# Kernel optimization log

Hardware: AMD Instinct MI355X
Metric: run time of the kernel (lower is better)

The kernel has to match this reference:

```python
import jax, jax.numpy as jnp
import numpy as np

D_IN = 256
H = 512


def _linear_params(key, fan_in, fan_out):
    kw, kb = jax.random.split(key)
    bound = 1.0 / np.sqrt(fan_in)
    W = jax.random.uniform(kw, (fan_in, fan_out), minval=-bound, maxval=bound, dtype=jnp.float32)
    b = jax.random.uniform(kb, (fan_out,), minval=-bound, maxval=bound, dtype=jnp.float32)
    return W, b


def setup_inputs() -> dict:
    key = jax.random.key(0)
    ks = jax.random.split(key, 7)
    brick_vectors = jax.random.normal(ks[0], (8, 128, D_IN), dtype=jnp.float32)
    Wa, ba = _linear_params(ks[1], D_IN, H)
    Wb, bb = _linear_params(ks[2], H, H)
    Wca, bca = _linear_params(ks[3], 2 * H, H)
    Wcb, bcb = _linear_params(ks[4], H, H)
    Wcc, bcc = _linear_params(ks[5], H, H)
    Wo, bo = _linear_params(ks[6], H, 2)
    return {
        "brick_vectors": brick_vectors,
        "Wa": Wa, "ba": ba,
        "Wb": Wb, "bb": bb,
        "Wca": Wca, "bca": bca,
        "Wcb": Wcb, "bcb": bcb,
        "Wcc": Wcc, "bcc": bcc,
        "Wo": Wo, "bo": bo,
    }


def reference(brick_vectors, Wa, ba, Wb, bb, Wca, bca, Wcb, bcb, Wcc, bcc, Wo, bo):
    B, N, _ = brick_vectors.shape
    x = brick_vectors.reshape(-1, D_IN)            # [B*N, D_IN]
    f = jax.nn.relu(x @ Wa + ba)                   # node MLP
    f = jax.nn.relu(f @ Wb + bb)                   # [B*N, 512]
    f = f.reshape(B, N, H)
    # pairwise broadcast-concat: pair (i, j) gets cat(f[:, j], f[:, i])
    fa = jnp.broadcast_to(f[:, None, :, :], (B, N, N, H))   # varies over j (last pair axis)
    fb = jnp.broadcast_to(f[:, :, None, :], (B, N, N, H))   # varies over i
    e = jnp.concatenate((fa, fb), axis=-1).reshape(-1, 2 * H)  # [B*N*N, 1024]
    e = jax.nn.relu(e @ Wca + bca)
    e = jax.nn.relu(e @ Wcb + bcb)
    e = jax.nn.relu(e @ Wcc + bcc)
    out = e @ Wo + bo                               # [B*N*N, 2]
    return out.reshape(B, N, N, 2)
```

## Files before the change

kernel.cpp:

```cpp
#include <hip/hip_runtime.h>

typedef __bf16 bf16x8 __attribute__((ext_vector_type(8)));
typedef float f32x16 __attribute__((ext_vector_type(16)));

#define GLOAD_LDS16(gsrc, ldst)                                                   \
  __builtin_amdgcn_global_load_lds(                                               \
      (const __attribute__((address_space(1))) void*)(gsrc),                      \
      (__attribute__((address_space(3))) void*)(ldst), 16, 0, 0)

__global__ __launch_bounds__(256) void prep_pack(const float* __restrict__ Wcb,
                                                 const float* __restrict__ Wcc,
                                                 __bf16* __restrict__ Pb,
                                                 __bf16* __restrict__ Pc) {
  int idx = blockIdx.x * 256 + threadIdx.x;
  const float* src = (idx < 262144) ? Wcb : Wcc;
  __bf16* dst = (idx < 262144) ? Pb : Pc;
  int t = idx & 262143;
  int e = t & 7, l = (t >> 3) & 63, kb = (t >> 9) & 31, c = t >> 14;
  int k = kb * 16 + ((l >> 5) << 3) + e;
  int n = (c << 5) + (l & 31);
  dst[t] = (__bf16)src[k * 512 + n];
}

__global__ __launch_bounds__(256) void gemm_f32(const float* __restrict__ A,
                                                const float* __restrict__ W,
                                                const float* __restrict__ bias,
                                                float* __restrict__ C,
                                                int K, int N, int do_relu) {
  __shared__ float As[16][68];
  __shared__ float Ws[16][32];
  int bm = blockIdx.x * 64, bn = blockIdx.y * 32;
  int tid = threadIdx.x;
  int tx = tid & 15, ty = tid >> 4;
  float acc[4][2] = {};
  for (int k0 = 0; k0 < K; k0 += 16) {
#pragma unroll
    for (int ii = 0; ii < 4; ii++) {
      int e = ii * 256 + tid; int r = e >> 4, c = e & 15;
      As[c][r] = A[(bm + r) * K + k0 + c];
    }
#pragma unroll
    for (int ii = 0; ii < 2; ii++) {
      int e = ii * 256 + tid; int kr = e >> 5, c = e & 31;
      Ws[kr][c] = W[(k0 + kr) * N + bn + c];
    }
    __syncthreads();
#pragma unroll
    for (int kk = 0; kk < 16; kk++) {
      float4 a = *(const float4*)&As[kk][ty * 4];
      float2 w = *(const float2*)&Ws[kk][tx * 2];
      acc[0][0] += a.x * w.x; acc[0][1] += a.x * w.y;
      acc[1][0] += a.y * w.x; acc[1][1] += a.y * w.y;
      acc[2][0] += a.z * w.x; acc[2][1] += a.z * w.y;
      acc[3][0] += a.w * w.x; acc[3][1] += a.w * w.y;
    }
    __syncthreads();
  }
#pragma unroll
  for (int mi = 0; mi < 4; mi++)
#pragma unroll
    for (int ni = 0; ni < 2; ni++) {
      int n = bn + tx * 2 + ni;
      float vv = acc[mi][ni] + (bias ? bias[n] : 0.f);
      if (do_relu) vv = fmaxf(vv, 0.f);
      C[(bm + ty * 4 + mi) * N + n] = vv;
    }
}

__global__ __launch_bounds__(256) void gemm_uv(const float* __restrict__ A,
                                               const float* __restrict__ Wca,
                                               float* __restrict__ u,
                                               float* __restrict__ v) {
  __shared__ float As[16][68];
  __shared__ float Ws[16][32];
  int half = blockIdx.y >> 4;
  const float* W = Wca + half * 512 * 512;
  float* C = half ? v : u;
  int bm = blockIdx.x * 64, bn = (blockIdx.y & 15) * 32;
  int tid = threadIdx.x;
  int tx = tid & 15, ty = tid >> 4;
  float acc[4][2] = {};
  for (int k0 = 0; k0 < 512; k0 += 16) {
#pragma unroll
    for (int ii = 0; ii < 4; ii++) {
      int e = ii * 256 + tid; int r = e >> 4, c = e & 15;
      As[c][r] = A[(bm + r) * 512 + k0 + c];
    }
#pragma unroll
    for (int ii = 0; ii < 2; ii++) {
      int e = ii * 256 + tid; int kr = e >> 5, c = e & 31;
      Ws[kr][c] = W[(k0 + kr) * 512 + bn + c];
    }
    __syncthreads();
#pragma unroll
    for (int kk = 0; kk < 16; kk++) {
      float4 a = *(const float4*)&As[kk][ty * 4];
      float2 w = *(const float2*)&Ws[kk][tx * 2];
      acc[0][0] += a.x * w.x; acc[0][1] += a.x * w.y;
      acc[1][0] += a.y * w.x; acc[1][1] += a.y * w.y;
      acc[2][0] += a.z * w.x; acc[2][1] += a.z * w.y;
      acc[3][0] += a.w * w.x; acc[3][1] += a.w * w.y;
    }
    __syncthreads();
  }
#pragma unroll
  for (int mi = 0; mi < 4; mi++)
#pragma unroll
    for (int ni = 0; ni < 2; ni++)
      C[(bm + ty * 4 + mi) * 512 + bn + tx * 2 + ni] = acc[mi][ni];
}

__global__ __launch_bounds__(512, 2) void edge_kernel(
    const float* __restrict__ u, const float* __restrict__ v,
    const bf16x8* __restrict__ Pb, const bf16x8* __restrict__ Pc,
    const float* __restrict__ bca, const float* __restrict__ bcb,
    const float* __restrict__ bcc, const float* __restrict__ Wo,
    const float* __restrict__ bo, float* __restrict__ out) {
  __shared__ __align__(16) char h_raw[163840];
  char* Bst = h_raw + 131072;

  int wg = blockIdx.x;
  int i = wg & 127, b = wg >> 7;
  int tid = threadIdx.x, lane = tid & 63, w = tid >> 6;

  int mrow = (w & 1) * 32;
  int n0 = (w >> 1) * 128;
  int cg4 = (w >> 1) * 4;
  int arow = mrow + (lane & 31);
  int sA = (arow & 15) << 4;
  int klo = (lane >> 5) * 8;
  int cb0 = 2 * w;

#define STAGE_B(P, kb, sel)                                                       \
  {                                                                               \
    const char* _g0 = (const char*)((P) + (cb0 * 32 + (kb)) * 64) + lane * 16;    \
    const char* _g1 = (const char*)((P) + ((cb0 + 1) * 32 + (kb)) * 64) + lane * 16; \
    GLOAD_LDS16(_g0, Bst + (sel) * 16384 + cb0 * 1024);                           \
    GLOAD_LDS16(_g1, Bst + (sel) * 16384 + (cb0 + 1) * 1024);                     \
  }

  STAGE_B(Pb, 0, 0)

  {
    int k2 = tid & 255;
    float2 vv = *(const float2*)(v + (b * 128 + i) * 512 + 2 * k2);
    float2 bc = *(const float2*)(bca + 2 * k2);
    float vb0 = vv.x + bc.x, vb1 = vv.y + bc.y;
    const float* ub = u + (b * 128) * 512;
#pragma unroll 4
    for (int it = 0; it < 64; it++) {
      int r = it * 2 + (tid >> 8);
      float2 uu = *(const float2*)(ub + r * 512 + 2 * k2);
      float x0 = fmaxf(uu.x + vb0, 0.f);
      float x1 = fmaxf(uu.y + vb1, 0.f);
      unsigned short s0 = __builtin_bit_cast(unsigned short, (__bf16)x0);
      unsigned short s1 = __builtin_bit_cast(unsigned short, (__bf16)x1);
      unsigned int pk = ((unsigned int)s1 << 16) | (unsigned int)s0;
      int rt = r & 63;
      int wbyte = ((r >> 6) << 16) + rt * 1024 + ((4 * k2) ^ ((rt & 15) << 4));
      *(unsigned int*)(h_raw + wbyte) = pk;
    }
  }
  __syncthreads();

  f32x16 acc0[4], acc1[4];

#pragma unroll
  for (int nb = 0; nb < 4; nb++)
#pragma unroll
    for (int r = 0; r < 16; r++) { acc0[nb][r] = 0.f; acc1[nb][r] = 0.f; }
#pragma unroll 2
  for (int kb = 0; kb < 32; kb++) {
    int sel = kb & 1;
    if (kb < 31) STAGE_B(Pb, kb + 1, sel ^ 1)
    const char* bb = Bst + sel * 16384 + lane * 16;
    bf16x8 b0 = *(const bf16x8*)(bb + (cg4 + 0) * 1024);
    bf16x8 b1 = *(const bf16x8*)(bb + (cg4 + 1) * 1024);
    bf16x8 b2 = *(const bf16x8*)(bb + (cg4 + 2) * 1024);
    bf16x8 b3 = *(const bf16x8*)(bb + (cg4 + 3) * 1024);
    int abyte = arow * 1024 + (((kb * 16 + klo) * 2) ^ sA);
    bf16x8 a0 = *(const bf16x8*)(h_raw + abyte);
    bf16x8 a1 = *(const bf16x8*)(h_raw + 65536 + abyte);
    acc0[0] = __builtin_amdgcn_mfma_f32_32x32x16_bf16(a0, b0, acc0[0], 0, 0, 0);
    acc1[0] = __builtin_amdgcn_mfma_f32_32x32x16_bf16(a1, b0, acc1[0], 0, 0, 0);
    acc0[1] = __builtin_amdgcn_mfma_f32_32x32x16_bf16(a0, b1, acc0[1], 0, 0, 0);
    acc1[1] = __builtin_amdgcn_mfma_f32_32x32x16_bf16(a1, b1, acc1[1], 0, 0, 0);
    acc0[2] = __builtin_amdgcn_mfma_f32_32x32x16_bf16(a0, b2, acc0[2], 0, 0, 0);
    acc1[2] = __builtin_amdgcn_mfma_f32_32x32x16_bf16(a1, b2, acc1[2], 0, 0, 0);
    acc0[3] = __builtin_amdgcn_mfma_f32_32x32x16_bf16(a0, b3, acc0[3], 0, 0, 0);
    acc1[3] = __builtin_amdgcn_mfma_f32_32x32x16_bf16(a1, b3, acc1[3], 0, 0, 0);
    __syncthreads();
  }
  STAGE_B(Pc, 0, 0)

#pragma unroll
  for (int nb = 0; nb < 4; nb++) {
    int cn = n0 + nb * 32 + (lane & 31);
    float bbv = bcb[cn];
#pragma unroll
    for (int r = 0; r < 16; r++) {
      int row = mrow + (r & 3) + 8 * (r >> 2) + 4 * (lane >> 5);
      int byte_ = row * 1024 + ((cn * 2) ^ ((row & 15) << 4));
      *(__bf16*)(h_raw + byte_) = (__bf16)fmaxf(acc0[nb][r] + bbv, 0.f);
      *(__bf16*)(h_raw + 65536 + byte_) = (__bf16)fmaxf(acc1[nb][r] + bbv, 0.f);
    }
  }
  __syncthreads();

#pragma unroll
  for (int nb = 0; nb < 4; nb++)
#pragma unroll
    for (int r = 0; r < 16; r++) { acc0[nb][r] = 0.f; acc1[nb][r] = 0.f; }
#pragma unroll 2
  for (int kb = 0; kb < 32; kb++) {
    int sel = kb & 1;
    if (kb < 31) STAGE_B(Pc, kb + 1, sel ^ 1)
    const char* bb = Bst + sel * 16384 + lane * 16;
    bf16x8 b0 = *(const bf16x8*)(bb + (cg4 + 0) * 1024);
    bf16x8 b1 = *(const bf16x8*)(bb + (cg4 + 1) * 1024);
    bf16x8 b2 = *(const bf16x8*)(bb + (cg4 + 2) * 1024);
    bf16x8 b3 = *(const bf16x8*)(bb + (cg4 + 3) * 1024);
    int abyte = arow * 1024 + (((kb * 16 + klo) * 2) ^ sA);
    bf16x8 a0 = *(const bf16x8*)(h_raw + abyte);
    bf16x8 a1 = *(const bf16x8*)(h_raw + 65536 + abyte);
    acc0[0] = __builtin_amdgcn_mfma_f32_32x32x16_bf16(a0, b0, acc0[0], 0, 0, 0);
    acc1[0] = __builtin_amdgcn_mfma_f32_32x32x16_bf16(a1, b0, acc1[0], 0, 0, 0);
    acc0[1] = __builtin_amdgcn_mfma_f32_32x32x16_bf16(a0, b1, acc0[1], 0, 0, 0);
    acc1[1] = __builtin_amdgcn_mfma_f32_32x32x16_bf16(a1, b1, acc1[1], 0, 0, 0);
    acc0[2] = __builtin_amdgcn_mfma_f32_32x32x16_bf16(a0, b2, acc0[2], 0, 0, 0);
    acc1[2] = __builtin_amdgcn_mfma_f32_32x32x16_bf16(a1, b2, acc1[2], 0, 0, 0);
    acc0[3] = __builtin_amdgcn_mfma_f32_32x32x16_bf16(a0, b3, acc0[3], 0, 0, 0);
    acc1[3] = __builtin_amdgcn_mfma_f32_32x32x16_bf16(a1, b3, acc1[3], 0, 0, 0);
    __syncthreads();
  }

  float p0[16][2] = {}, p1[16][2] = {};
#pragma unroll
  for (int nb = 0; nb < 4; nb++) {
    int cn = n0 + nb * 32 + (lane & 31);
    float bcv = bcc[cn];
    float2 wov = *(const float2*)(Wo + cn * 2);
#pragma unroll
    for (int r = 0; r < 16; r++) {
      float h30 = fmaxf(acc0[nb][r] + bcv, 0.f);
      float h31 = fmaxf(acc1[nb][r] + bcv, 0.f);
      p0[r][0] += h30 * wov.x; p0[r][1] += h30 * wov.y;
      p1[r][0] += h31 * wov.x; p1[r][1] += h31 * wov.y;
    }
  }
#pragma unroll
  for (int m = 1; m <= 16; m <<= 1) {
#pragma unroll
    for (int r = 0; r < 16; r++) {
      p0[r][0] += __shfl_xor(p0[r][0], m, 64);
      p0[r][1] += __shfl_xor(p0[r][1], m, 64);
      p1[r][0] += __shfl_xor(p1[r][0], m, 64);
      p1[r][1] += __shfl_xor(p1[r][1], m, 64);
    }
  }
  __syncthreads();
  float* red = (float*)h_raw;
  if ((lane & 31) == 0) {
    int hh = lane >> 5, cg = w >> 1;
#pragma unroll
    for (int r = 0; r < 16; r++) {
      int row = mrow + (r & 3) + 8 * (r >> 2) + 4 * hh;
      red[(cg * 128 + row) * 2 + 0] = p0[r][0];
      red[(cg * 128 + row) * 2 + 1] = p0[r][1];
      red[(cg * 128 + 64 + row) * 2 + 0] = p1[r][0];
      red[(cg * 128 + 64 + row) * 2 + 1] = p1[r][1];
    }
  }
  __syncthreads();
  if (tid < 256) {
    int row = tid >> 1, d = tid & 1;
    float s = red[(0 * 128 + row) * 2 + d] + red[(1 * 128 + row) * 2 + d] +
              red[(2 * 128 + row) * 2 + d] + red[(3 * 128 + row) * 2 + d] + bo[d];
    out[((b * 128 + i) * 128 + row) * 2 + d] = s;
  }
#undef STAGE_B
}

extern "C" void kernel_launch(void* const* d_in, const int* in_sizes, int n_in,
                              void* d_out, int out_size, void* d_ws, size_t ws_size,
                              hipStream_t stream) {
  const float* x   = (const float*)d_in[0];
  const float* Wa  = (const float*)d_in[1];
  const float* ba  = (const float*)d_in[2];
  const float* Wb  = (const float*)d_in[3];
  const float* bb  = (const float*)d_in[4];
  const float* Wca = (const float*)d_in[5];
  const float* bca = (const float*)d_in[6];
  const float* Wcb = (const float*)d_in[7];
  const float* bcb = (const float*)d_in[8];
  const float* Wcc = (const float*)d_in[9];
  const float* bcc = (const float*)d_in[10];
  const float* Wo  = (const float*)d_in[11];
  const float* bo  = (const float*)d_in[12];
  float* out = (float*)d_out;

  char* ws = (char*)d_ws;
  float* f1 = (float*)(ws);
  float* f  = (float*)(ws + (2u << 20));
  float* u  = (float*)(ws + (4u << 20));
  float* v  = (float*)(ws + (6u << 20));
  __bf16* Pb = (__bf16*)(ws + (8u << 20));
  __bf16* Pc = (__bf16*)(ws + (8u << 20) + (512u << 10));

  prep_pack<<<2048, 256, 0, stream>>>(Wcb, Wcc, Pb, Pc);
  gemm_f32<<<dim3(16, 16), 256, 0, stream>>>(x, Wa, ba, f1, 256, 512, 1);
  gemm_f32<<<dim3(16, 16), 256, 0, stream>>>(f1, Wb, bb, f, 512, 512, 1);
  gemm_uv<<<dim3(16, 32), 256, 0, stream>>>(f, Wca, u, v);
  edge_kernel<<<1024, 512, 0, stream>>>(u, v, (const bf16x8*)Pb, (const bf16x8*)Pc,
                                        bca, bcb, bcc, Wo, bo, out);
}
```

Before: 255.6 us.

## Split edge tiles to 64 rows, 4-slot B prefetch with fine-grained waitcnt

Each workgroup now handles 64 j-rows instead of 128, doubling the grid to 2048 blocks and shrinking LDS use from 160KB to 128KB. Each wave now owns 64 output columns (two 32-wide blocks) rather than 128, so it holds four accumulators instead of eight. Weight staging moves to a 4-slot ring with a prefetch distance of two, explicit vmcnt waits and raw s_barrier instead of __syncthreads, and s_setprio around the MFMAs. This targets the per-k-step sync stalls and aims for better latency hiding. The cost is that each block streams the full weight matrices for only half the rows, which doubles weight traffic per output.

```diff
diff --git a/kernel.cpp b/kernel.cpp
--- a/kernel.cpp
+++ b/kernel.cpp
@@ -116,39 +116,54 @@
     const float* __restrict__ bca, const float* __restrict__ bcb,
     const float* __restrict__ bcc, const float* __restrict__ Wo,
     const float* __restrict__ bo, float* __restrict__ out) {
-  __shared__ __align__(16) char h_raw[163840];
-  char* Bst = h_raw + 131072;
+  __shared__ __align__(16) char h_raw[131072];
+  char* Bst = h_raw + 65536;
 
   int wg = blockIdx.x;
-  int i = wg & 127, b = wg >> 7;
+  int jh = wg & 1, i = (wg >> 1) & 127, b = wg >> 8;
+  int j0 = jh * 64;
   int tid = threadIdx.x, lane = tid & 63, w = tid >> 6;
 
-  int mrow = (w & 1) * 32;
-  int n0 = (w >> 1) * 128;
-  int cg4 = (w >> 1) * 4;
-  int arow = mrow + (lane & 31);
-  int sA = (arow & 15) << 4;
+  int cb0 = 2 * w;
+  int r0 = lane & 31;
+  int sA = (r0 & 15) << 4;
   int klo = (lane >> 5) * 8;
-  int cb0 = 2 * w;
-
-#define STAGE_B(P, kb, sel)                                                       \
+
+#define STAGE_B(P, kb, slot)                                                      \
   {                                                                               \
-    const char* _g0 = (const char*)((P) + (cb0 * 32 + (kb)) * 64) + lane * 16;    \
-    const char* _g1 = (const char*)((P) + ((cb0 + 1) * 32 + (kb)) * 64) + lane * 16; \
-    GLOAD_LDS16(_g0, Bst + (sel) * 16384 + cb0 * 1024);                           \
-    GLOAD_LDS16(_g1, Bst + (sel) * 16384 + (cb0 + 1) * 1024);                     \
-  }
-
-  STAGE_B(Pb, 0, 0)
+    const char* g0_ = (const char*)((P) + ((cb0) * 32 + (kb)) * 64) + lane * 16;  \
+    const char* g1_ = (const char*)((P) + ((cb0 + 1) * 32 + (kb)) * 64) + lane * 16; \
+    GLOAD_LDS16(g0_, Bst + (slot) * 16384 + (cb0) * 1024);                        \
+    GLOAD_LDS16(g1_, Bst + (slot) * 16384 + (cb0 + 1) * 1024);                    \
+  }
+
+#define KSTEP(P, kb, DO_STAGE, VMSTR)                                             \
+  {                                                                               \
+    if (DO_STAGE) STAGE_B(P, (kb) + 2, ((kb) + 2) & 3)                            \
+    const char* bb_ = Bst + ((kb) & 3) * 16384 + lane * 16;                       \
+    bf16x8 b0 = *(const bf16x8*)(bb_ + cb0 * 1024);                               \
+    bf16x8 b1 = *(const bf16x8*)(bb_ + (cb0 + 1) * 1024);                         \
+    int ab_ = (((kb) * 16 + klo) * 2) ^ sA;                                       \
+    bf16x8 a0 = *(const bf16x8*)(h_raw + r0 * 1024 + ab_);                        \
+    bf16x8 a1 = *(const bf16x8*)(h_raw + (r0 + 32) * 1024 + ab_);                 \
+    __builtin_amdgcn_s_setprio(1);                                                \
+    accA0 = __builtin_amdgcn_mfma_f32_32x32x16_bf16(a0, b0, accA0, 0, 0, 0);      \
+    accA1 = __builtin_amdgcn_mfma_f32_32x32x16_bf16(a0, b1, accA1, 0, 0, 0);      \
+    accB0 = __builtin_amdgcn_mfma_f32_32x32x16_bf16(a1, b0, accB0, 0, 0, 0);      \
+    accB1 = __builtin_amdgcn_mfma_f32_32x32x16_bf16(a1, b1, accB1, 0, 0, 0);      \
+    __builtin_amdgcn_s_setprio(0);                                                \
+    asm volatile("s_waitcnt vmcnt(" VMSTR ")" ::: "memory");                      \
+    __builtin_amdgcn_s_barrier();                                                 \
+  }
 
   {
     int k2 = tid & 255;
     float2 vv = *(const float2*)(v + (b * 128 + i) * 512 + 2 * k2);
     float2 bc = *(const float2*)(bca + 2 * k2);
     float vb0 = vv.x + bc.x, vb1 = vv.y + bc.y;
-    const float* ub = u + (b * 128) * 512;
+    const float* ub = u + (b * 128 + j0) * 512;
 #pragma unroll 4
-    for (int it = 0; it < 64; it++) {
+    for (int it = 0; it < 32; it++) {
       int r = it * 2 + (tid >> 8);
       float2 uu = *(const float2*)(ub + r * 512 + 2 * k2);
       float x0 = fmaxf(uu.x + vb0, 0.f);
@@ -156,94 +171,63 @@
       unsigned short s0 = __builtin_bit_cast(unsigned short, (__bf16)x0);
       unsigned short s1 = __builtin_bit_cast(unsigned short, (__bf16)x1);
       unsigned int pk = ((unsigned int)s1 << 16) | (unsigned int)s0;
-      int rt = r & 63;
-      int wbyte = ((r >> 6) << 16) + rt * 1024 + ((4 * k2) ^ ((rt & 15) << 4));
+      int wbyte = r * 1024 + ((4 * k2) ^ ((r & 15) << 4));
       *(unsigned int*)(h_raw + wbyte) = pk;
     }
   }
-  __syncthreads();
-
-  f32x16 acc0[4], acc1[4];
-
-#pragma unroll
-  for (int nb = 0; nb < 4; nb++)
-#pragma unroll
-    for (int r = 0; r < 16; r++) { acc0[nb][r] = 0.f; acc1[nb][r] = 0.f; }
-#pragma unroll 2
-  for (int kb = 0; kb < 32; kb++) {
-    int sel = kb & 1;
-    if (kb < 31) STAGE_B(Pb, kb + 1, sel ^ 1)
-    const char* bb = Bst + sel * 16384 + lane * 16;
-    bf16x8 b0 = *(const bf16x8*)(bb + (cg4 + 0) * 1024);
-    bf16x8 b1 = *(const bf16x8*)(bb + (cg4 + 1) * 1024);
-    bf16x8 b2 = *(const bf16x8*)(bb + (cg4 + 2) * 1024);
-    bf16x8 b3 = *(const bf16x8*)(bb + (cg4 + 3) * 1024);
-    int abyte = arow * 1024 + (((kb * 16 + klo) * 2) ^ sA);
-    bf16x8 a0 = *(const bf16x8*)(h_raw + abyte);
-    bf16x8 a1 = *(const bf16x8*)(h_raw + 65536 + abyte);
-    acc0[0] = __builtin_amdgcn_mfma_f32_32x32x16_bf16(a0, b0, acc0[0], 0, 0, 0);
-    acc1[0] = __builtin_amdgcn_mfma_f32_32x32x16_bf16(a1, b0, acc1[0], 0, 0, 0);
-    acc0[1] = __builtin_amdgcn_mfma_f32_32x32x16_bf16(a0, b1, acc0[1], 0, 0, 0);
-    acc1[1] = __builtin_amdgcn_mfma_f32_32x32x16_bf16(a1, b1, acc1[1], 0, 0, 0);
-    acc0[2] = __builtin_amdgcn_mfma_f32_32x32x16_bf16(a0, b2, acc0[2], 0, 0, 0);
-    acc1[2] = __builtin_amdgcn_mfma_f32_32x32x16_bf16(a1, b2, acc1[2], 0, 0, 0);
-    acc0[3] = __builtin_amdgcn_mfma_f32_32x32x16_bf16(a0, b3, acc0[3], 0, 0, 0);
-    acc1[3] = __builtin_amdgcn_mfma_f32_32x32x16_bf16(a1, b3, acc1[3], 0, 0, 0);
-    __syncthreads();
-  }
+
+  f32x16 accA0, accA1, accB0, accB1;
+#pragma unroll
+  for (int r = 0; r < 16; r++) { accA0[r] = 0.f; accA1[r] = 0.f; accB0[r] = 0.f; accB1[r] = 0.f; }
+
+  asm volatile("s_waitcnt vmcnt(0)" ::: "memory");
+  STAGE_B(Pb, 0, 0)
+  STAGE_B(Pb, 1, 1)
+  asm volatile("s_waitcnt vmcnt(2) lgkmcnt(0)" ::: "memory");
+  __builtin_amdgcn_s_barrier();
+
+  for (int kb = 0; kb < 30; kb++) KSTEP(Pb, kb, 1, "2")
+  KSTEP(Pb, 30, 0, "0")
+  KSTEP(Pb, 31, 0, "0")
+
   STAGE_B(Pc, 0, 0)
-
-#pragma unroll
-  for (int nb = 0; nb < 4; nb++) {
-    int cn = n0 + nb * 32 + (lane & 31);
+  STAGE_B(Pc, 1, 1)
+
+#pragma unroll
+  for (int blk = 0; blk < 2; blk++) {
+    int cn = (cb0 + blk) * 32 + (lane & 31);
     float bbv = bcb[cn];
+    const f32x16& A0 = blk ? accA1 : accA0;
+    const f32x16& A1 = blk ? accB1 : accB0;
 #pragma unroll
     for (int r = 0; r < 16; r++) {
-      int row = mrow + (r & 3) + 8 * (r >> 2) + 4 * (lane >> 5);
-      int byte_ = row * 1024 + ((cn * 2) ^ ((row & 15) << 4));
-      *(__bf16*)(h_raw + byte_) = (__bf16)fmaxf(acc0[nb][r] + bbv, 0.f);
-      *(__bf16*)(h_raw + 65536 + byte_) = (__bf16)fmaxf(acc1[nb][r] + bbv, 0.f);
-    }
-  }
-  __syncthreads();
-
-#pragma unroll
-  for (int nb = 0; nb < 4; nb++)
-#pragma unroll
-    for (int r = 0; r < 16; r++) { acc0[nb][r] = 0.f; acc1[nb][r] = 0.f; }
-#pragma unroll 2
-  for (int kb = 0; kb < 32; kb++) {
-    int sel = kb & 1;
-    if (kb < 31) STAGE_B(Pc, kb + 1, sel ^ 1)
-    const char* bb = Bst + sel * 16384 + lane * 16;
-    bf16x8 b0 = *(const bf16x8*)(bb + (cg4 + 0) * 1024);
-    bf16x8 b1 = *(const bf16x8*)(bb + (cg4 + 1) * 1024);
-    bf16x8 b2 = *(const bf16x8*)(bb + (cg4 + 2) * 1024);
-    bf16x8 b3 = *(const bf16x8*)(bb + (cg4 + 3) * 1024);
-    int abyte = arow * 1024 + (((kb * 16 + klo) * 2) ^ sA);
-    bf16x8 a0 = *(const bf16x8*)(h_raw + abyte);
-    bf16x8 a1 = *(const bf16x8*)(h_raw + 65536 + abyte);
-    acc0[0] = __builtin_amdgcn_mfma_f32_32x32x16_bf16(a0, b0, acc0[0], 0, 0, 0);
-    acc1[0] = __builtin_amdgcn_mfma_f32_32x32x16_bf16(a1, b0, acc1[0], 0, 0, 0);
-    acc0[1] = __builtin_amdgcn_mfma_f32_32x32x16_bf16(a0, b1, acc0[1], 0, 0, 0);
-    acc1[1] = __builtin_amdgcn_mfma_f32_32x32x16_bf16(a1, b1, acc1[1], 0, 0, 0);
-    acc0[2] = __builtin_amdgcn_mfma_f32_32x32x16_bf16(a0, b2, acc0[2], 0, 0, 0);
-    acc1[2] = __builtin_amdgcn_mfma_f32_32x32x16_bf16(a1, b2, acc1[2], 0, 0, 0);
-    acc0[3] = __builtin_amdgcn_mfma_f32_32x32x16_bf16(a0, b3, acc0[3], 0, 0, 0);
-    acc1[3] = __builtin_amdgcn_mfma_f32_32x32x16_bf16(a1, b3, acc1[3], 0, 0, 0);
-    __syncthreads();
-  }
+      int crow = (r & 3) + 8 * (r >> 2) + 4 * (lane >> 5);
+      int byte_ = crow * 1024 + ((cn * 2) ^ ((crow & 15) << 4));
+      *(__bf16*)(h_raw + byte_) = (__bf16)fmaxf(A0[r] + bbv, 0.f);
+      *(__bf16*)(h_raw + byte_ + 32 * 1024) = (__bf16)fmaxf(A1[r] + bbv, 0.f);
+    }
+  }
+#pragma unroll
+  for (int r = 0; r < 16; r++) { accA0[r] = 0.f; accA1[r] = 0.f; accB0[r] = 0.f; accB1[r] = 0.f; }
+  asm volatile("s_waitcnt vmcnt(2) lgkmcnt(0)" ::: "memory");
+  __builtin_amdgcn_s_barrier();
+
+  for (int kb = 0; kb < 30; kb++) KSTEP(Pc, kb, 1, "2")
+  KSTEP(Pc, 30, 0, "0")
+  KSTEP(Pc, 31, 0, "0")
 
   float p0[16][2] = {}, p1[16][2] = {};
 #pragma unroll
-  for (int nb = 0; nb < 4; nb++) {
-    int cn = n0 + nb * 32 + (lane & 31);
+  for (int blk = 0; blk < 2; blk++) {
+    int cn = (cb0 + blk) * 32 + (lane & 31);
     float bcv = bcc[cn];
     float2 wov = *(const float2*)(Wo + cn * 2);
+    const f32x16& A0 = blk ? accA1 : accA0;
+    const f32x16& A1 = blk ? accB1 : accB0;
 #pragma unroll
     for (int r = 0; r < 16; r++) {
-      float h30 = fmaxf(acc0[nb][r] + bcv, 0.f);
-      float h31 = fmaxf(acc1[nb][r] + bcv, 0.f);
+      float h30 = fmaxf(A0[r] + bcv, 0.f);
+      float h31 = fmaxf(A1[r] + bcv, 0.f);
       p0[r][0] += h30 * wov.x; p0[r][1] += h30 * wov.y;
       p1[r][0] += h31 * wov.x; p1[r][1] += h31 * wov.y;
     }
@@ -261,23 +245,25 @@
   __syncthreads();
   float* red = (float*)h_raw;
   if ((lane & 31) == 0) {
-    int hh = lane >> 5, cg = w >> 1;
+    int hh = lane >> 5;
 #pragma unroll
     for (int r = 0; r < 16; r++) {
-      int row = mrow + (r & 3) + 8 * (r >> 2) + 4 * hh;
-      red[(cg * 128 + row) * 2 + 0] = p0[r][0];
-      red[(cg * 128 + row) * 2 + 1] = p0[r][1];
-      red[(cg * 128 + 64 + row) * 2 + 0] = p1[r][0];
-      red[(cg * 128 + 64 + row) * 2 + 1] = p1[r][1];
+      int crow = (r & 3) + 8 * (r >> 2) + 4 * hh;
+      red[(w * 64 + crow) * 2 + 0] = p0[r][0];
+      red[(w * 64 + crow) * 2 + 1] = p0[r][1];
+      red[(w * 64 + 32 + crow) * 2 + 0] = p1[r][0];
+      red[(w * 64 + 32 + crow) * 2 + 1] = p1[r][1];
     }
   }
   __syncthreads();
-  if (tid < 256) {
+  if (tid < 128) {
     int row = tid >> 1, d = tid & 1;
-    float s = red[(0 * 128 + row) * 2 + d] + red[(1 * 128 + row) * 2 + d] +
-              red[(2 * 128 + row) * 2 + d] + red[(3 * 128 + row) * 2 + d] + bo[d];
-    out[((b * 128 + i) * 128 + row) * 2 + d] = s;
-  }
+    float s = bo[d];
+#pragma unroll
+    for (int ww = 0; ww < 8; ww++) s += red[(ww * 64 + row) * 2 + d];
+    out[(((b * 128 + i) * 128) + j0 + row) * 2 + d] = s;
+  }
+#undef KSTEP
 #undef STAGE_B
 }
 
@@ -311,6 +297,6 @@
   gemm_f32<<<dim3(16, 16), 256, 0, stream>>>(x, Wa, ba, f1, 256, 512, 1);
   gemm_f32<<<dim3(16, 16), 256, 0, stream>>>(f1, Wb, bb, f, 512, 512, 1);
   gemm_uv<<<dim3(16, 32), 256, 0, stream>>>(f, Wca, u, v);
-  edge_kernel<<<1024, 512, 0, stream>>>(u, v, (const bf16x8*)Pb, (const bf16x8*)Pc,
+  edge_kernel<<<2048, 512, 0, stream>>>(u, v, (const bf16x8*)Pb, (const bf16x8*)Pc,
                                         bca, bcb, bcc, Wo, bo, out);
 }
```

Measured after the change: 302.5 us. 1.18x slower.

## Replace scalar fp32 node GEMMs with bf16 MFMA kernels using packed weights

Applied to the files above, without the earlier changes.

The three fp32 SIMT GEMMs for the node MLP and the u/v projection are replaced by a templated bf16 MFMA kernel. It stages activations into swizzled LDS and reads weights prepacked into MFMA fragment order. All weight packing now happens in one larger pack kernel. This cuts per-node GEMM compute time but only launches 16–32 blocks of 512 threads, and lowers node-feature precision to bf16.

```diff
diff --git a/kernel.cpp b/kernel.cpp
--- a/kernel.cpp
+++ b/kernel.cpp
@@ -8,106 +8,115 @@
       (const __attribute__((address_space(1))) void*)(gsrc),                      \
       (__attribute__((address_space(3))) void*)(ldst), 16, 0, 0)
 
-__global__ __launch_bounds__(256) void prep_pack(const float* __restrict__ Wcb,
-                                                 const float* __restrict__ Wcc,
-                                                 __bf16* __restrict__ Pb,
-                                                 __bf16* __restrict__ Pc) {
-  int idx = blockIdx.x * 256 + threadIdx.x;
-  const float* src = (idx < 262144) ? Wcb : Wcc;
-  __bf16* dst = (idx < 262144) ? Pb : Pc;
-  int t = idx & 262143;
-  int e = t & 7, l = (t >> 3) & 63, kb = (t >> 9) & 31, c = t >> 14;
+__device__ __forceinline__ void pack_one(const float* __restrict__ src,
+                                         __bf16* __restrict__ dst,
+                                         int t, int kbshift) {
+  int e = t & 7, l = (t >> 3) & 63;
+  int kb = (t >> 9) & ((1 << kbshift) - 1);
+  int c = t >> (9 + kbshift);
   int k = kb * 16 + ((l >> 5) << 3) + e;
   int n = (c << 5) + (l & 31);
   dst[t] = (__bf16)src[k * 512 + n];
 }
 
-__global__ __launch_bounds__(256) void gemm_f32(const float* __restrict__ A,
-                                                const float* __restrict__ W,
-                                                const float* __restrict__ bias,
-                                                float* __restrict__ C,
-                                                int K, int N, int do_relu) {
-  __shared__ float As[16][68];
-  __shared__ float Ws[16][32];
-  int bm = blockIdx.x * 64, bn = blockIdx.y * 32;
-  int tid = threadIdx.x;
-  int tx = tid & 15, ty = tid >> 4;
-  float acc[4][2] = {};
-  for (int k0 = 0; k0 < K; k0 += 16) {
-#pragma unroll
-    for (int ii = 0; ii < 4; ii++) {
-      int e = ii * 256 + tid; int r = e >> 4, c = e & 15;
-      As[c][r] = A[(bm + r) * K + k0 + c];
-    }
-#pragma unroll
-    for (int ii = 0; ii < 2; ii++) {
-      int e = ii * 256 + tid; int kr = e >> 5, c = e & 31;
-      Ws[kr][c] = W[(k0 + kr) * N + bn + c];
-    }
-    __syncthreads();
-#pragma unroll
-    for (int kk = 0; kk < 16; kk++) {
-      float4 a = *(const float4*)&As[kk][ty * 4];
-      float2 w = *(const float2*)&Ws[kk][tx * 2];
-      acc[0][0] += a.x * w.x; acc[0][1] += a.x * w.y;
-      acc[1][0] += a.y * w.x; acc[1][1] += a.y * w.y;
-      acc[2][0] += a.z * w.x; acc[2][1] += a.z * w.y;
-      acc[3][0] += a.w * w.x; acc[3][1] += a.w * w.y;
-    }
-    __syncthreads();
-  }
-#pragma unroll
-  for (int mi = 0; mi < 4; mi++)
-#pragma unroll
-    for (int ni = 0; ni < 2; ni++) {
-      int n = bn + tx * 2 + ni;
-      float vv = acc[mi][ni] + (bias ? bias[n] : 0.f);
-      if (do_relu) vv = fmaxf(vv, 0.f);
-      C[(bm + ty * 4 + mi) * N + n] = vv;
-    }
-}
-
-__global__ __launch_bounds__(256) void gemm_uv(const float* __restrict__ A,
-                                               const float* __restrict__ Wca,
-                                               float* __restrict__ u,
-                                               float* __restrict__ v) {
-  __shared__ float As[16][68];
-  __shared__ float Ws[16][32];
-  int half = blockIdx.y >> 4;
-  const float* W = Wca + half * 512 * 512;
-  float* C = half ? v : u;
-  int bm = blockIdx.x * 64, bn = (blockIdx.y & 15) * 32;
-  int tid = threadIdx.x;
-  int tx = tid & 15, ty = tid >> 4;
-  float acc[4][2] = {};
-  for (int k0 = 0; k0 < 512; k0 += 16) {
-#pragma unroll
-    for (int ii = 0; ii < 4; ii++) {
-      int e = ii * 256 + tid; int r = e >> 4, c = e & 15;
-      As[c][r] = A[(bm + r) * 512 + k0 + c];
-    }
-#pragma unroll
-    for (int ii = 0; ii < 2; ii++) {
-      int e = ii * 256 + tid; int kr = e >> 5, c = e & 31;
-      Ws[kr][c] = W[(k0 + kr) * 512 + bn + c];
-    }
-    __syncthreads();
-#pragma unroll
-    for (int kk = 0; kk < 16; kk++) {
-      float4 a = *(const float4*)&As[kk][ty * 4];
-      float2 w = *(const float2*)&Ws[kk][tx * 2];
-      acc[0][0] += a.x * w.x; acc[0][1] += a.x * w.y;
-      acc[1][0] += a.y * w.x; acc[1][1] += a.y * w.y;
-      acc[2][0] += a.z * w.x; acc[2][1] += a.z * w.y;
-      acc[3][0] += a.w * w.x; acc[3][1] += a.w * w.y;
-    }
-    __syncthreads();
-  }
-#pragma unroll
-  for (int mi = 0; mi < 4; mi++)
-#pragma unroll
-    for (int ni = 0; ni < 2; ni++)
-      C[(bm + ty * 4 + mi) * 512 + bn + tx * 2 + ni] = acc[mi][ni];
+__global__ __launch_bounds__(256) void pack_all(
+    const float* __restrict__ Wcb, const float* __restrict__ Wcc,
+    const float* __restrict__ Wb, const float* __restrict__ Wca,
+    const float* __restrict__ Wa,
+    __bf16* __restrict__ Pb, __bf16* __restrict__ Pc,
+    __bf16* __restrict__ PWb, __bf16* __restrict__ PH0,
+    __bf16* __restrict__ PH1, __bf16* __restrict__ PWa) {
+  int idx = blockIdx.x * 256 + threadIdx.x;
+  if (idx < 262144) {
+    pack_one(Wcb, Pb, idx, 5);
+  } else if (idx < 524288) {
+    pack_one(Wcc, Pc, idx - 262144, 5);
+  } else if (idx < 786432) {
+    pack_one(Wb, PWb, idx - 524288, 5);
+  } else if (idx < 1048576) {
+    pack_one(Wca, PH0, idx - 786432, 5);
+  } else if (idx < 1310720) {
+    pack_one(Wca + 512 * 512, PH1, idx - 1048576, 5);
+  } else if (idx < 1441792) {
+    pack_one(Wa, PWa, idx - 1310720, 4);
+  }
+}
+
+template <int K>
+__global__ __launch_bounds__(512, 2) void node_mfma(
+    const float* __restrict__ A, const bf16x8* __restrict__ P0,
+    const bf16x8* __restrict__ P1, const float* __restrict__ bias,
+    int do_relu, float* __restrict__ C0, float* __restrict__ C1) {
+  constexpr int KB = K / 16;
+  constexpr int KH = K / 2;
+  __shared__ __align__(16) char sA[64 * K * 2];
+
+  int row0 = blockIdx.x * 64;
+  const bf16x8* P = blockIdx.y ? P1 : P0;
+  float* C = blockIdx.y ? C1 : C0;
+  int tid = threadIdx.x, lane = tid & 63, w = tid >> 6;
+
+  {
+    int k2 = tid & (KH - 1);
+    int rof = tid / KH;
+    constexpr int RPI = 512 / KH;
+#pragma unroll 4
+    for (int it = 0; it < 64 / RPI; it++) {
+      int r = it * RPI + rof;
+      float2 aa = *(const float2*)(A + (row0 + r) * K + 2 * k2);
+      unsigned short s0 = __builtin_bit_cast(unsigned short, (__bf16)aa.x);
+      unsigned short s1 = __builtin_bit_cast(unsigned short, (__bf16)aa.y);
+      unsigned int pk = ((unsigned int)s1 << 16) | (unsigned int)s0;
+      int wbyte = r * (2 * K) + ((4 * k2) ^ ((r & 15) << 4));
+      *(unsigned int*)(sA + wbyte) = pk;
+    }
+  }
+  __syncthreads();
+
+  int mrow = (w & 1) * 32;
+  int n0 = (w >> 1) * 128;
+  int cg4 = (w >> 1) * 4;
+  int arow = mrow + (lane & 31);
+  int sAk = (arow & 15) << 4;
+  int klo = (lane >> 5) * 8;
+
+  const bf16x8* B0 = P + ((cg4 + 0) * KB) * 64 + lane;
+  const bf16x8* B1 = P + ((cg4 + 1) * KB) * 64 + lane;
+  const bf16x8* B2 = P + ((cg4 + 2) * KB) * 64 + lane;
+  const bf16x8* B3 = P + ((cg4 + 3) * KB) * 64 + lane;
+
+  f32x16 acc[4];
+#pragma unroll
+  for (int nb = 0; nb < 4; nb++)
+#pragma unroll
+    for (int r = 0; r < 16; r++) acc[nb][r] = 0.f;
+
+#pragma unroll 2
+  for (int kb = 0; kb < KB; kb++) {
+    int abyte = arow * (2 * K) + (((kb * 16 + klo) * 2) ^ sAk);
+    bf16x8 a = *(const bf16x8*)(sA + abyte);
+    bf16x8 b0 = B0[kb * 64];
+    bf16x8 b1 = B1[kb * 64];
+    bf16x8 b2 = B2[kb * 64];
+    bf16x8 b3 = B3[kb * 64];
+    acc[0] = __builtin_amdgcn_mfma_f32_32x32x16_bf16(a, b0, acc[0], 0, 0, 0);
+    acc[1] = __builtin_amdgcn_mfma_f32_32x32x16_bf16(a, b1, acc[1], 0, 0, 0);
+    acc[2] = __builtin_amdgcn_mfma_f32_32x32x16_bf16(a, b2, acc[2], 0, 0, 0);
+    acc[3] = __builtin_amdgcn_mfma_f32_32x32x16_bf16(a, b3, acc[3], 0, 0, 0);
+  }
+
+#pragma unroll
+  for (int nb = 0; nb < 4; nb++) {
+    int cn = n0 + nb * 32 + (lane & 31);
+    float bv = bias ? bias[cn] : 0.f;
+#pragma unroll
+    for (int r = 0; r < 16; r++) {
+      int rr = mrow + (r & 3) + 8 * (r >> 2) + 4 * (lane >> 5);
+      float val = acc[nb][r] + bv;
+      if (do_relu) val = fmaxf(val, 0.f);
+      C[(row0 + rr) * 512 + cn] = val;
+    }
+  }
 }
 
 __global__ __launch_bounds__(512, 2) void edge_kernel(
@@ -304,13 +313,21 @@
   float* f  = (float*)(ws + (2u << 20));
   float* u  = (float*)(ws + (4u << 20));
   float* v  = (float*)(ws + (6u << 20));
-  __bf16* Pb = (__bf16*)(ws + (8u << 20));
-  __bf16* Pc = (__bf16*)(ws + (8u << 20) + (512u << 10));
-
-  prep_pack<<<2048, 256, 0, stream>>>(Wcb, Wcc, Pb, Pc);
-  gemm_f32<<<dim3(16, 16), 256, 0, stream>>>(x, Wa, ba, f1, 256, 512, 1);
-  gemm_f32<<<dim3(16, 16), 256, 0, stream>>>(f1, Wb, bb, f, 512, 512, 1);
-  gemm_uv<<<dim3(16, 32), 256, 0, stream>>>(f, Wca, u, v);
+  __bf16* Pb  = (__bf16*)(ws + (8u << 20));
+  __bf16* Pc  = (__bf16*)(ws + (8u << 20) + (512u << 10));
+  __bf16* PWb = (__bf16*)(ws + (9u << 20));
+  __bf16* PH0 = (__bf16*)(ws + (9u << 20) + (512u << 10));
+  __bf16* PH1 = (__bf16*)(ws + (10u << 20));
+  __bf16* PWa = (__bf16*)(ws + (10u << 20) + (512u << 10));
+
+  pack_all<<<5632, 256, 0, stream>>>(Wcb, Wcc, Wb, Wca, Wa,
+                                     Pb, Pc, PWb, PH0, PH1, PWa);
+  node_mfma<256><<<dim3(16, 1), 512, 0, stream>>>(
+      x, (const bf16x8*)PWa, (const bf16x8*)PWa, ba, 1, f1, f1);
+  node_mfma<512><<<dim3(16, 1), 512, 0, stream>>>(
+      f1, (const bf16x8*)PWb, (const bf16x8*)PWb, bb, 1, f, f);
+  node_mfma<512><<<dim3(16, 2), 512, 0, stream>>>(
+      f, (const bf16x8*)PH0, (const bf16x8*)PH1, nullptr, 0, u, v);
   edge_kernel<<<1024, 512, 0, stream>>>(u, v, (const bf16x8*)Pb, (const bf16x8*)Pc,
                                         bca, bcb, bcc, Wo, bo, out);
 }
```

New measurement: 231.2 us. -9.5%, faster.
